# Performance work log

Measured on AMD Instinct MI355X. Metric: run time of the kernel, lower is better.

Reference implementation:

```python
import math
import jax, jax.numpy as jnp
import numpy as np

B, L, D, H, DFF = 2, 2048, 1024, 16, 4096
HD = D // H
NUM_BUCKETS, MAX_DISTANCE = 32, 128


def setup_inputs() -> dict:
    key = jax.random.key(0)
    ks = jax.random.split(key, 10)
    s = 0.02
    return {
        "hidden_states": jax.random.normal(ks[0], (B, L, D), dtype=jnp.float32),
        "Wq": jax.random.normal(ks[1], (D, D), dtype=jnp.float32) * s,
        "Wk": jax.random.normal(ks[2], (D, D), dtype=jnp.float32) * s,
        "Wv": jax.random.normal(ks[3], (D, D), dtype=jnp.float32) * s,
        "Wo": jax.random.normal(ks[4], (D, D), dtype=jnp.float32) * s,
        "W1": jax.random.normal(ks[5], (D, DFF), dtype=jnp.float32) * s,
        "W2": jax.random.normal(ks[6], (DFF, D), dtype=jnp.float32) * s,
        "ln1_g": jnp.ones((D,), dtype=jnp.float32),
        "ln2_g": jnp.ones((D,), dtype=jnp.float32),
        "rel_table": jax.random.normal(ks[7], (NUM_BUCKETS, H), dtype=jnp.float32) * s,
    }


def rms_norm(x, g, eps=1e-6):
    # T5-style LayerNorm: scale only, no mean subtraction
    var = jnp.mean(jnp.square(x.astype(jnp.float32)), axis=-1, keepdims=True)
    return (x.astype(jnp.float32) * jax.lax.rsqrt(var + eps)).astype(x.dtype) * g


def relative_position_bias(seq_len, table):
    # bidirectional T5 bucket scheme, num_buckets=32, max_distance=128
    ctx = jnp.arange(seq_len)[:, None]
    mem = jnp.arange(seq_len)[None, :]
    rp = mem - ctx                                  # (L, L) int
    nb = NUM_BUCKETS // 2
    buckets = (rp > 0).astype(jnp.int32) * nb
    rpa = jnp.abs(rp)
    max_exact = nb // 2
    is_small = rpa < max_exact
    safe = jnp.maximum(rpa, 1).astype(jnp.float32)  # avoid log(0); masked by is_small
    large = max_exact + (
        jnp.log(safe / max_exact) / math.log(MAX_DISTANCE / max_exact) * (nb - max_exact)
    ).astype(jnp.int32)
    large = jnp.minimum(large, nb - 1)
    buckets = buckets + jnp.where(is_small, rpa, large)   # (L, L)
    vals = table[buckets]                                  # (L, L, H)
    return jnp.transpose(vals, (2, 0, 1))[None]            # (1, H, L, L)


def reference(hidden_states, Wq, Wk, Wv, Wo, W1, W2, ln1_g, ln2_g, rel_table):
    x = hidden_states
    b, l, d = x.shape

    # --- self-attention sublayer (pre-norm) ---
    h = rms_norm(x, ln1_g)
    q = (h @ Wq).reshape(b, l, H, HD)
    k = (h @ Wk).reshape(b, l, H, HD)
    v = (h @ Wv).reshape(b, l, H, HD)

    bias = relative_position_bias(l, rel_table)            # (1, H, L, L)
    # NOTE: source's manual attention path has NO 1/sqrt(head_dim) scaling
    scores = jnp.einsum("bqhd,bkhd->bhqk", q, k) + bias
    attn = jax.nn.softmax(scores.astype(jnp.float32), axis=-1).astype(scores.dtype)
    out = jnp.einsum("bhqk,bkhd->bqhd", attn, v).reshape(b, l, d)
    x = x + out @ Wo

    # --- feed-forward sublayer (pre-norm) ---
    h = rms_norm(x, ln2_g)
    x = x + jax.nn.relu(h @ W1) @ W2
    return x
```

## Files before the change

kernel.cpp:

```cpp
#include <hip/hip_runtime.h>
#include <hip/hip_bf16.h>
#include <math.h>

#define BDIM 1024
#define HEADS 16
#define HDIM 64
#define LSEQ 2048
#define NBATCH 2
#define DFFDIM 4096
#define QKVN 3072

typedef __bf16 bf16x8_t __attribute__((ext_vector_type(8)));
typedef float f32x4_t __attribute__((ext_vector_type(4)));

__device__ __forceinline__ ushort f2bf(float f) {
    union { __hip_bfloat16 b; ushort u; } cv;
    cv.b = __float2bfloat16(f);
    return cv.u;
}
__device__ __forceinline__ float bf2f(ushort u) {
    union { unsigned int i; float f; } cv;
    cv.i = ((unsigned int)u) << 16;
    return cv.f;
}

__global__ __launch_bounds__(256) void transpose_cvt(const float* __restrict__ W,
                                                     ushort* __restrict__ Wt,
                                                     int K, int N) {
    __shared__ ushort tile[32][33];
    int bi = blockIdx.y;
    int bj = blockIdx.x;
    int tx = threadIdx.x;
    int ty = threadIdx.y;
#pragma unroll
    for (int r = 0; r < 4; ++r) {
        int krow = bi * 32 + ty + r * 8;
        int ncol = bj * 32 + tx;
        tile[ty + r * 8][tx] = f2bf(W[(size_t)krow * N + ncol]);
    }
    __syncthreads();
#pragma unroll
    for (int r = 0; r < 4; ++r) {
        int nrow = bj * 32 + ty + r * 8;
        int kcol = bi * 32 + tx;
        Wt[(size_t)nrow * K + kcol] = tile[tx][ty + r * 8];
    }
}

__global__ __launch_bounds__(256) void vtrans(const ushort* __restrict__ qkv,
                                              ushort* __restrict__ vT) {
    __shared__ ushort t[64][72];
    const int ktile = blockIdx.x;
    const int bh = blockIdx.y;
    const int b = bh >> 4, h = bh & 15;
    const int tid = threadIdx.x;
    const int r = tid >> 2;
    const int c0 = (tid & 3) * 16;
    const ushort* src = qkv + (size_t)(b * LSEQ + ktile * 64 + r) * QKVN + 2048 + h * HDIM + c0;
    union { bf16x8_t v; ushort s[8]; } u0, u1;
    u0.v = *(const bf16x8_t*)src;
    u1.v = *(const bf16x8_t*)(src + 8);
#pragma unroll
    for (int j = 0; j < 8; ++j) { t[r][c0 + j] = u0.s[j]; t[r][c0 + 8 + j] = u1.s[j]; }
    __syncthreads();
    const int hd = tid >> 2;
    union { bf16x8_t v; ushort s[8]; } w0, w1;
#pragma unroll
    for (int j = 0; j < 8; ++j) { w0.s[j] = t[c0 + j][hd]; w1.s[j] = t[c0 + 8 + j][hd]; }
    ushort* dst = vT + (size_t)(bh * HDIM + hd) * LSEQ + ktile * 64 + c0;
    *(bf16x8_t*)dst = w0.v;
    *(bf16x8_t*)(dst + 8) = w1.v;
}

__global__ __launch_bounds__(256) void rmsnorm_k(const float* __restrict__ x,
                                                 const float* __restrict__ g,
                                                 ushort* __restrict__ out) {
    int row = blockIdx.x;
    int t = threadIdx.x;
    int w = t >> 6, l = t & 63;
    const float4 v = reinterpret_cast<const float4*>(x + (size_t)row * BDIM)[t];
    float ss = v.x * v.x + v.y * v.y + v.z * v.z + v.w * v.w;
#pragma unroll
    for (int m = 1; m <= 32; m <<= 1) ss += __shfl_xor(ss, m);
    __shared__ float wsum[4];
    if (l == 0) wsum[w] = ss;
    __syncthreads();
    float tot = wsum[0] + wsum[1] + wsum[2] + wsum[3];
    float r = rsqrtf(tot * (1.0f / BDIM) + 1e-6f);
    const float4 gv = reinterpret_cast<const float4*>(g)[t];
    ushort4 o;
    o.x = f2bf(v.x * r * gv.x);
    o.y = f2bf(v.y * r * gv.y);
    o.z = f2bf(v.z * r * gv.z);
    o.w = f2bf(v.w * r * gv.w);
    reinterpret_cast<ushort4*>(out + (size_t)row * BDIM)[t] = o;
}

__global__ void bias_table_k(const float* __restrict__ rel, float* __restrict__ btab) {
    int idx = blockIdx.x * 256 + threadIdx.x;
    if (idx >= HEADS * 4095) return;
    int h = idx / 4095;
    int d = idx % 4095;
    int rp = d - 2047;
    int bucket = rp > 0 ? 16 : 0;
    int rpa = rp < 0 ? -rp : rp;
    if (rpa < 8) {
        bucket += rpa;
    } else {
        int large = 8 + (int)(logf((float)rpa * 0.125f) * (1.0f / logf(16.0f)) * 8.0f);
        bucket += large < 15 ? large : 15;
    }
    btab[idx] = rel[bucket * HEADS + h];
}

__global__ __launch_bounds__(256) void reduce2_k(const ushort* __restrict__ parts,
                                                 const float* __restrict__ res,
                                                 float* __restrict__ out,
                                                 size_t mn) {
    size_t i = ((size_t)blockIdx.x * 256 + threadIdx.x) * 4;
    float4 r = *(const float4*)(res + i);
    ushort4 a = *(const ushort4*)(parts + i);
    ushort4 b = *(const ushort4*)(parts + mn + i);
    float4 o;
    o.x = r.x + bf2f(a.x) + bf2f(b.x);
    o.y = r.y + bf2f(a.y) + bf2f(b.y);
    o.z = r.z + bf2f(a.z) + bf2f(b.z);
    o.w = r.w + bf2f(a.w) + bf2f(b.w);
    *(float4*)(out + i) = o;
}

template <int MODE, int TM, int TN>
__global__ __launch_bounds__(256) void gemm_bt(const ushort* __restrict__ A,
                                               const ushort* __restrict__ Bt,
                                               void* Cout, const float* res,
                                               int M, int N, int K, int nbx, int nkc) {
    __shared__ __align__(16) ushort As[2][TM * 64];
    __shared__ __align__(16) ushort Bs[2][TN * 64];
    constexpr int MF = TM / 32, NF = TN / 32;
    const int nwg = gridDim.x;
    const int bid = blockIdx.x;
    const int swz = (bid & 7) * (nwg >> 3) + (bid >> 3);
    const int nxy = nwg / nkc;
    const int chunk = swz / nxy;
    const int bxy = swz % nxy;
    const int bx = bxy % nbx, by = bxy / nbx;
    const int Kc = K / nkc;
    const int kbeg = chunk * Kc;
    const int tid = threadIdx.x;
    const int w = tid >> 6, l = tid & 63;
    const int wm = w >> 1, wn = w & 1;
    const int rowA0 = by * TM;
    const int colB0 = bx * TN;
    const int lr = l >> 3;
    const int scs = ((l & 7) ^ lr) * 8;
    const int c = l & 15, gq = l >> 4;
    const int rswz = (c & 7) * 8;
    f32x4_t acc[MF][NF] = {};

    auto stage = [&](int buf, int k0) {
#pragma unroll
        for (int i = 0; i < TM / 32; ++i) {
            int r = i * 32 + w * 8;
            __builtin_amdgcn_global_load_lds(
                (const __attribute__((address_space(1))) uint32_t*)(A + (size_t)(rowA0 + r + lr) * K + kbeg + k0 + scs),
                (__attribute__((address_space(3))) uint32_t*)(&As[buf][r * 64]), 16, 0, 0);
        }
#pragma unroll
        for (int i = 0; i < TN / 32; ++i) {
            int r = i * 32 + w * 8;
            __builtin_amdgcn_global_load_lds(
                (const __attribute__((address_space(1))) uint32_t*)(Bt + (size_t)(colB0 + r + lr) * K + kbeg + k0 + scs),
                (__attribute__((address_space(3))) uint32_t*)(&Bs[buf][r * 64]), 16, 0, 0);
        }
    };

    stage(0, 0);
    int cur = 0;
    const int nk = Kc >> 6;
    for (int kt = 0; kt < nk; ++kt) {
        __syncthreads();
        if (kt + 1 < nk) stage(cur ^ 1, (kt + 1) << 6);
#pragma unroll
        for (int kk = 0; kk < 2; ++kk) {
            bf16x8_t av[MF], bv[NF];
#pragma unroll
            for (int mf = 0; mf < MF; ++mf)
                av[mf] = *(const bf16x8_t*)&As[cur][(wm * (TM / 2) + mf * 16 + c) * 64 + ((kk * 32 + gq * 8) ^ rswz)];
#pragma unroll
            for (int nf = 0; nf < NF; ++nf)
                bv[nf] = *(const bf16x8_t*)&Bs[cur][(wn * (TN / 2) + nf * 16 + c) * 64 + ((kk * 32 + gq * 8) ^ rswz)];
#pragma unroll
            for (int mf = 0; mf < MF; ++mf)
#pragma unroll
                for (int nf = 0; nf < NF; ++nf)
                    acc[mf][nf] = __builtin_amdgcn_mfma_f32_16x16x32_bf16(av[mf], bv[nf], acc[mf][nf], 0, 0, 0);
        }
        cur ^= 1;
    }
#pragma unroll
    for (int mf = 0; mf < MF; ++mf) {
#pragma unroll
        for (int nf = 0; nf < NF; ++nf) {
#pragma unroll
            for (int i = 0; i < 4; ++i) {
                int row = rowA0 + wm * (TM / 2) + mf * 16 + gq * 4 + i;
                int col = colB0 + wn * (TN / 2) + nf * 16 + c;
                size_t idx = (size_t)row * N + col;
                float vv = acc[mf][nf][i];
                if (MODE == 0) {
                    ((ushort*)Cout)[idx] = f2bf(vv);
                } else if (MODE == 1) {
                    ((float*)Cout)[idx] = res[idx] + vv;
                } else if (MODE == 2) {
                    ((ushort*)Cout)[idx] = f2bf(vv > 0.f ? vv : 0.f);
                } else {
                    ((ushort*)Cout)[(size_t)chunk * M * N + idx] = f2bf(vv);
                }
            }
        }
    }
}

__global__ __launch_bounds__(512) void attn_fwd(const ushort* __restrict__ qkv,
                                                const ushort* __restrict__ vT,
                                                const float* __restrict__ btab,
                                                ushort* __restrict__ ob) {
    const int tid = threadIdx.x, w = tid >> 6, l = tid & 63;
    const int bh = blockIdx.y, b = bh >> 4, h = bh & 15;
    const int qt = blockIdx.x;
    __shared__ __align__(16) ushort Ks[2][64 * 64];
    __shared__ __align__(16) ushort Vs[2][64 * 64];
    __shared__ __align__(16) ushort Pl[8][16 * 72];
    const int q0 = qt * 128 + w * 16;
    const int c = l & 15, g = l >> 4;
    const size_t rowbase = (size_t)b * LSEQ * QKVN;
    const ushort* qp = qkv + rowbase + h * HDIM;
    const ushort* kp = qkv + rowbase + BDIM + h * HDIM;
    const ushort* vtp = vT + (size_t)bh * HDIM * LSEQ;
    const int sr = tid >> 3;
    const int scs = ((l & 7) ^ (l >> 3)) * 8;
    const float* btq4 = btab + h * 4095 + 2047 - (q0 + c) + g * 4;

    bf16x8_t aq[2];
#pragma unroll
    for (int kk = 0; kk < 2; ++kk)
        aq[kk] = *(const bf16x8_t*)(qp + (size_t)(q0 + c) * QKVN + kk * 32 + g * 8);

    float mrow = -INFINITY, lrow = 0.f;
    f32x4_t o[4] = {};
    f32x4_t s[4];

    auto stage = [&](int buf, int key0) {
        __builtin_amdgcn_global_load_lds(
            (const __attribute__((address_space(1))) uint32_t*)(kp + (size_t)(key0 + sr) * QKVN + scs),
            (__attribute__((address_space(3))) uint32_t*)(&Ks[buf][(w * 8) * 64]), 16, 0, 0);
        __builtin_amdgcn_global_load_lds(
            (const __attribute__((address_space(1))) uint32_t*)(vtp + (size_t)sr * LSEQ + key0 + scs),
            (__attribute__((address_space(3))) uint32_t*)(&Vs[buf][(w * 8) * 64]), 16, 0, 0);
    };
    auto loadBias = [&](int key0) {
#pragma unroll
        for (int nf = 0; nf < 4; ++nf)
#pragma unroll
            for (int i = 0; i < 4; ++i)
                s[nf][i] = btq4[key0 + nf * 16 + i];
    };

    stage(0, 0);
    loadBias(0);
    int cur = 0;

    ushort* Pw = Pl[w];
    const int rswz = (c & 7) << 3;
    for (int kt = 0; kt < 32; ++kt) {
        __syncthreads();
        if (kt < 31) stage(cur ^ 1, kt * 64 + 64);
#pragma unroll
        for (int kk = 0; kk < 2; ++kk)
#pragma unroll
            for (int nf = 0; nf < 4; ++nf) {
                bf16x8_t kf = *(const bf16x8_t*)&Ks[cur][(nf * 16 + c) * 64 + ((kk * 32 + g * 8) ^ rswz)];
                s[nf] = __builtin_amdgcn_mfma_f32_16x16x32_bf16(kf, aq[kk], s[nf], 0, 0, 0);
            }
        float tmax = -INFINITY;
#pragma unroll
        for (int nf = 0; nf < 4; ++nf)
#pragma unroll
            for (int i = 0; i < 4; ++i)
                tmax = fmaxf(tmax, s[nf][i]);
        tmax = fmaxf(tmax, __shfl_xor(tmax, 16));
        tmax = fmaxf(tmax, __shfl_xor(tmax, 32));
        if (!__all(tmax - mrow <= 8.f)) {
            float mn = fmaxf(mrow, tmax);
            float sc2 = __expf(mrow - mn);
            mrow = mn;
            lrow *= sc2;
#pragma unroll
            for (int hf = 0; hf < 4; ++hf) o[hf] *= sc2;
        }
        float rs = 0.f;
        union { ushort us[4]; uint2 u2; } pk[4];
#pragma unroll
        for (int nf = 0; nf < 4; ++nf)
#pragma unroll
            for (int i = 0; i < 4; ++i) {
                float pv = __expf(s[nf][i] - mrow);
                rs += pv;
                pk[nf].us[i] = f2bf(pv);
            }
        if (kt < 31) loadBias(kt * 64 + 64);
        rs += __shfl_xor(rs, 16);
        rs += __shfl_xor(rs, 32);
        lrow += rs;
#pragma unroll
        for (int nf = 0; nf < 4; ++nf)
            *(uint2*)&Pw[c * 72 + nf * 16 + g * 4] = pk[nf].u2;
        bf16x8_t pa[2];
#pragma unroll
        for (int kk = 0; kk < 2; ++kk)
            pa[kk] = *(const bf16x8_t*)&Pw[c * 72 + kk * 32 + g * 8];
#pragma unroll
        for (int kk = 0; kk < 2; ++kk)
#pragma unroll
            for (int hf = 0; hf < 4; ++hf) {
                bf16x8_t vf = *(const bf16x8_t*)&Vs[cur][(hf * 16 + c) * 64 + ((kk * 32 + g * 8) ^ rswz)];
                o[hf] = __builtin_amdgcn_mfma_f32_16x16x32_bf16(vf, pa[kk], o[hf], 0, 0, 0);
            }
        cur ^= 1;
    }
    const float inv = 1.f / lrow;
    ushort* orow = ob + (size_t)(b * LSEQ + q0 + c) * BDIM + h * HDIM + g * 4;
#pragma unroll
    for (int hf = 0; hf < 4; ++hf) {
        ushort4 ov;
        ov.x = f2bf(o[hf][0] * inv);
        ov.y = f2bf(o[hf][1] * inv);
        ov.z = f2bf(o[hf][2] * inv);
        ov.w = f2bf(o[hf][3] * inv);
        *(ushort4*)(orow + hf * 16) = ov;
    }
}

extern "C" void kernel_launch(void* const* d_in, const int* in_sizes, int n_in,
                              void* d_out, int out_size, void* d_ws, size_t ws_size,
                              hipStream_t stream) {
    const float* x   = (const float*)d_in[0];
    const float* Wq  = (const float*)d_in[1];
    const float* Wk  = (const float*)d_in[2];
    const float* Wv  = (const float*)d_in[3];
    const float* Wo  = (const float*)d_in[4];
    const float* W1  = (const float*)d_in[5];
    const float* W2  = (const float*)d_in[6];
    const float* g1  = (const float*)d_in[7];
    const float* g2  = (const float*)d_in[8];
    const float* rel = (const float*)d_in[9];
    float* out = (float*)d_out;

    char* ws = (char*)d_ws;
    const size_t MB = 1024 * 1024;
    ushort* wqkvT = (ushort*)(ws + 0 * MB);
    ushort* woT   = (ushort*)(ws + 6 * MB);
    ushort* w1T   = (ushort*)(ws + 8 * MB);
    ushort* w2T   = (ushort*)(ws + 16 * MB);
    float*  btab  = (float*)(ws + 24 * MB);
    ushort* hbuf  = (ushort*)(ws + 25 * MB);
    ushort* qkvb  = (ushort*)(ws + 33 * MB);
    ushort* woP   = (ushort*)(ws + 33 * MB);
    ushort* f1b   = (ushort*)(ws + 33 * MB);
    ushort* vTb   = (ushort*)(ws + 57 * MB);
    ushort* w2P   = (ushort*)(ws + 0 * MB);
    (void)in_sizes; (void)n_in; (void)out_size; (void)ws_size;

    const size_t MN = (size_t)4096 * 1024;
    dim3 tb(32, 8);
    transpose_cvt<<<dim3(32, 32),  tb, 0, stream>>>(Wq, wqkvT,                1024, 1024);
    transpose_cvt<<<dim3(32, 32),  tb, 0, stream>>>(Wk, wqkvT + 1024 * 1024,  1024, 1024);
    transpose_cvt<<<dim3(32, 32),  tb, 0, stream>>>(Wv, wqkvT + 2048 * 1024,  1024, 1024);
    transpose_cvt<<<dim3(32, 32),  tb, 0, stream>>>(Wo, woT, 1024, 1024);
    transpose_cvt<<<dim3(128, 32), tb, 0, stream>>>(W1, w1T, 1024, 4096);
    transpose_cvt<<<dim3(32, 128), tb, 0, stream>>>(W2, w2T, 4096, 1024);
    bias_table_k<<<256, 256, 0, stream>>>(rel, btab);

    rmsnorm_k<<<4096, 256, 0, stream>>>(x, g1, hbuf);
    gemm_bt<0, 128, 64><<<1536, 256, 0, stream>>>(hbuf, wqkvT, qkvb, nullptr, 4096, QKVN, 1024, 48, 1);
    vtrans<<<dim3(32, 32), 256, 0, stream>>>(qkvb, vTb);
    attn_fwd<<<dim3(16, 32), 512, 0, stream>>>(qkvb, vTb, btab, hbuf);
    gemm_bt<3, 128, 64><<<1024, 256, 0, stream>>>(hbuf, woT, woP, nullptr, 4096, 1024, 1024, 16, 2);
    reduce2_k<<<4096, 256, 0, stream>>>(woP, x, out, MN);
    rmsnorm_k<<<4096, 256, 0, stream>>>(out, g2, hbuf);
    gemm_bt<2, 128, 64><<<2048, 256, 0, stream>>>(hbuf, w1T, f1b, nullptr, 4096, DFFDIM, 1024, 64, 1);
    gemm_bt<3, 128, 64><<<1024, 256, 0, stream>>>(f1b, w2T, w2P, nullptr, 4096, 1024, 4096, 16, 2);
    reduce2_k<<<4096, 256, 0, stream>>>(w2P, out, out, MN);
}
```

Measured before the change: 276.8 us.

## Enlarge GEMM tiles, single-buffer LDS, fuse residual+RMSNorm, tune attention softmax

Switches all GEMMs to 128x128 tiles with a single LDS buffer and two barriers per K step, dropping the double-buffered prefetch. The residual reduction is fused with the second RMSNorm into one kernel, removing a pass over the activations. The attention kernel gains s_setprio hints around its MFMA blocks, a tree max reduction, and exp2-based softmax with a prescaled max. The larger tiles are meant to increase data reuse per block, but they lower occupancy, and the single buffer exposes global-load latency that prefetching used to hide.

Result: faster. 259.6 us (-6.2%).

```diff
diff --git a/kernel.cpp b/kernel.cpp
--- a/kernel.cpp
+++ b/kernel.cpp
@@ -9,6 +9,7 @@
 #define NBATCH 2
 #define DFFDIM 4096
 #define QKVN 3072
+#define LOG2E 1.44269504f
 
 typedef __bf16 bf16x8_t __attribute__((ext_vector_type(8)));
 typedef float f32x4_t __attribute__((ext_vector_type(4)));
@@ -129,13 +130,49 @@
     *(float4*)(out + i) = o;
 }
 
+__global__ __launch_bounds__(256) void reduce2_rms(const ushort* __restrict__ parts,
+                                                   const float* __restrict__ res,
+                                                   const float* __restrict__ g,
+                                                   float* __restrict__ out,
+                                                   ushort* __restrict__ hout,
+                                                   size_t mn) {
+    int row = blockIdx.x;
+    int t = threadIdx.x;
+    int w = t >> 6, l = t & 63;
+    size_t i = (size_t)row * BDIM + t * 4;
+    float4 r = *(const float4*)(res + i);
+    ushort4 a = *(const ushort4*)(parts + i);
+    ushort4 b = *(const ushort4*)(parts + mn + i);
+    float4 o;
+    o.x = r.x + bf2f(a.x) + bf2f(b.x);
+    o.y = r.y + bf2f(a.y) + bf2f(b.y);
+    o.z = r.z + bf2f(a.z) + bf2f(b.z);
+    o.w = r.w + bf2f(a.w) + bf2f(b.w);
+    *(float4*)(out + i) = o;
+    float ss = o.x * o.x + o.y * o.y + o.z * o.z + o.w * o.w;
+#pragma unroll
+    for (int m = 1; m <= 32; m <<= 1) ss += __shfl_xor(ss, m);
+    __shared__ float wsum[4];
+    if (l == 0) wsum[w] = ss;
+    __syncthreads();
+    float tot = wsum[0] + wsum[1] + wsum[2] + wsum[3];
+    float rr = rsqrtf(tot * (1.0f / BDIM) + 1e-6f);
+    const float4 gv = reinterpret_cast<const float4*>(g)[t];
+    ushort4 h;
+    h.x = f2bf(o.x * rr * gv.x);
+    h.y = f2bf(o.y * rr * gv.y);
+    h.z = f2bf(o.z * rr * gv.z);
+    h.w = f2bf(o.w * rr * gv.w);
+    reinterpret_cast<ushort4*>(hout + (size_t)row * BDIM)[t] = h;
+}
+
 template <int MODE, int TM, int TN>
 __global__ __launch_bounds__(256) void gemm_bt(const ushort* __restrict__ A,
                                                const ushort* __restrict__ Bt,
                                                void* Cout, const float* res,
                                                int M, int N, int K, int nbx, int nkc) {
-    __shared__ __align__(16) ushort As[2][TM * 64];
-    __shared__ __align__(16) ushort Bs[2][TN * 64];
+    __shared__ __align__(16) ushort As[TM * 64];
+    __shared__ __align__(16) ushort Bs[TN * 64];
     constexpr int MF = TM / 32, NF = TN / 32;
     const int nwg = gridDim.x;
     const int bid = blockIdx.x;
@@ -157,45 +194,43 @@
     const int rswz = (c & 7) * 8;
     f32x4_t acc[MF][NF] = {};
 
-    auto stage = [&](int buf, int k0) {
+    auto stage = [&](int k0) {
 #pragma unroll
         for (int i = 0; i < TM / 32; ++i) {
             int r = i * 32 + w * 8;
             __builtin_amdgcn_global_load_lds(
                 (const __attribute__((address_space(1))) uint32_t*)(A + (size_t)(rowA0 + r + lr) * K + kbeg + k0 + scs),
-                (__attribute__((address_space(3))) uint32_t*)(&As[buf][r * 64]), 16, 0, 0);
+                (__attribute__((address_space(3))) uint32_t*)(&As[r * 64]), 16, 0, 0);
         }
 #pragma unroll
         for (int i = 0; i < TN / 32; ++i) {
             int r = i * 32 + w * 8;
             __builtin_amdgcn_global_load_lds(
                 (const __attribute__((address_space(1))) uint32_t*)(Bt + (size_t)(colB0 + r + lr) * K + kbeg + k0 + scs),
-                (__attribute__((address_space(3))) uint32_t*)(&Bs[buf][r * 64]), 16, 0, 0);
+                (__attribute__((address_space(3))) uint32_t*)(&Bs[r * 64]), 16, 0, 0);
         }
     };
 
-    stage(0, 0);
-    int cur = 0;
     const int nk = Kc >> 6;
     for (int kt = 0; kt < nk; ++kt) {
         __syncthreads();
-        if (kt + 1 < nk) stage(cur ^ 1, (kt + 1) << 6);
+        stage(kt << 6);
+        __syncthreads();
 #pragma unroll
         for (int kk = 0; kk < 2; ++kk) {
             bf16x8_t av[MF], bv[NF];
 #pragma unroll
             for (int mf = 0; mf < MF; ++mf)
-                av[mf] = *(const bf16x8_t*)&As[cur][(wm * (TM / 2) + mf * 16 + c) * 64 + ((kk * 32 + gq * 8) ^ rswz)];
+                av[mf] = *(const bf16x8_t*)&As[(wm * (TM / 2) + mf * 16 + c) * 64 + ((kk * 32 + gq * 8) ^ rswz)];
 #pragma unroll
             for (int nf = 0; nf < NF; ++nf)
-                bv[nf] = *(const bf16x8_t*)&Bs[cur][(wn * (TN / 2) + nf * 16 + c) * 64 + ((kk * 32 + gq * 8) ^ rswz)];
+                bv[nf] = *(const bf16x8_t*)&Bs[(wn * (TN / 2) + nf * 16 + c) * 64 + ((kk * 32 + gq * 8) ^ rswz)];
 #pragma unroll
             for (int mf = 0; mf < MF; ++mf)
 #pragma unroll
                 for (int nf = 0; nf < NF; ++nf)
                     acc[mf][nf] = __builtin_amdgcn_mfma_f32_16x16x32_bf16(av[mf], bv[nf], acc[mf][nf], 0, 0, 0);
         }
-        cur ^= 1;
     }
 #pragma unroll
     for (int mf = 0; mf < MF; ++mf) {
@@ -246,7 +281,7 @@
     for (int kk = 0; kk < 2; ++kk)
         aq[kk] = *(const bf16x8_t*)(qp + (size_t)(q0 + c) * QKVN + kk * 32 + g * 8);
 
-    float mrow = -INFINITY, lrow = 0.f;
+    float mrow = -INFINITY, lrow = 0.f, m2 = -INFINITY;
     f32x4_t o[4] = {};
     f32x4_t s[4];
 
@@ -275,6 +310,7 @@
     for (int kt = 0; kt < 32; ++kt) {
         __syncthreads();
         if (kt < 31) stage(cur ^ 1, kt * 64 + 64);
+        __builtin_amdgcn_s_setprio(1);
 #pragma unroll
         for (int kk = 0; kk < 2; ++kk)
 #pragma unroll
@@ -282,18 +318,19 @@
                 bf16x8_t kf = *(const bf16x8_t*)&Ks[cur][(nf * 16 + c) * 64 + ((kk * 32 + g * 8) ^ rswz)];
                 s[nf] = __builtin_amdgcn_mfma_f32_16x16x32_bf16(kf, aq[kk], s[nf], 0, 0, 0);
             }
-        float tmax = -INFINITY;
-#pragma unroll
-        for (int nf = 0; nf < 4; ++nf)
-#pragma unroll
-            for (int i = 0; i < 4; ++i)
-                tmax = fmaxf(tmax, s[nf][i]);
+        __builtin_amdgcn_s_setprio(0);
+        float tmax = fmaxf(
+            fmaxf(fmaxf(fmaxf(s[0][0], s[0][1]), fmaxf(s[0][2], s[0][3])),
+                  fmaxf(fmaxf(s[1][0], s[1][1]), fmaxf(s[1][2], s[1][3]))),
+            fmaxf(fmaxf(fmaxf(s[2][0], s[2][1]), fmaxf(s[2][2], s[2][3])),
+                  fmaxf(fmaxf(s[3][0], s[3][1]), fmaxf(s[3][2], s[3][3]))));
         tmax = fmaxf(tmax, __shfl_xor(tmax, 16));
         tmax = fmaxf(tmax, __shfl_xor(tmax, 32));
         if (!__all(tmax - mrow <= 8.f)) {
             float mn = fmaxf(mrow, tmax);
-            float sc2 = __expf(mrow - mn);
+            float sc2 = exp2f((mrow - mn) * LOG2E);
             mrow = mn;
+            m2 = mn * LOG2E;
             lrow *= sc2;
 #pragma unroll
             for (int hf = 0; hf < 4; ++hf) o[hf] *= sc2;
@@ -304,7 +341,7 @@
         for (int nf = 0; nf < 4; ++nf)
 #pragma unroll
             for (int i = 0; i < 4; ++i) {
-                float pv = __expf(s[nf][i] - mrow);
+                float pv = exp2f(fmaf(s[nf][i], LOG2E, -m2));
                 rs += pv;
                 pk[nf].us[i] = f2bf(pv);
             }
@@ -319,6 +356,7 @@
 #pragma unroll
         for (int kk = 0; kk < 2; ++kk)
             pa[kk] = *(const bf16x8_t*)&Pw[c * 72 + kk * 32 + g * 8];
+        __builtin_amdgcn_s_setprio(1);
 #pragma unroll
         for (int kk = 0; kk < 2; ++kk)
 #pragma unroll
@@ -326,6 +364,7 @@
                 bf16x8_t vf = *(const bf16x8_t*)&Vs[cur][(hf * 16 + c) * 64 + ((kk * 32 + g * 8) ^ rswz)];
                 o[hf] = __builtin_amdgcn_mfma_f32_16x16x32_bf16(vf, pa[kk], o[hf], 0, 0, 0);
             }
+        __builtin_amdgcn_s_setprio(0);
         cur ^= 1;
     }
     const float inv = 1.f / lrow;
@@ -382,13 +421,12 @@
     bias_table_k<<<256, 256, 0, stream>>>(rel, btab);
 
     rmsnorm_k<<<4096, 256, 0, stream>>>(x, g1, hbuf);
-    gemm_bt<0, 128, 64><<<1536, 256, 0, stream>>>(hbuf, wqkvT, qkvb, nullptr, 4096, QKVN, 1024, 48, 1);
+    gemm_bt<0, 128, 128><<<768, 256, 0, stream>>>(hbuf, wqkvT, qkvb, nullptr, 4096, QKVN, 1024, 24, 1);
     vtrans<<<dim3(32, 32), 256, 0, stream>>>(qkvb, vTb);
     attn_fwd<<<dim3(16, 32), 512, 0, stream>>>(qkvb, vTb, btab, hbuf);
-    gemm_bt<3, 128, 64><<<1024, 256, 0, stream>>>(hbuf, woT, woP, nullptr, 4096, 1024, 1024, 16, 2);
-    reduce2_k<<<4096, 256, 0, stream>>>(woP, x, out, MN);
-    rmsnorm_k<<<4096, 256, 0, stream>>>(out, g2, hbuf);
-    gemm_bt<2, 128, 64><<<2048, 256, 0, stream>>>(hbuf, w1T, f1b, nullptr, 4096, DFFDIM, 1024, 64, 1);
-    gemm_bt<3, 128, 64><<<1024, 256, 0, stream>>>(f1b, w2T, w2P, nullptr, 4096, 1024, 4096, 16, 2);
+    gemm_bt<3, 128, 128><<<512, 256, 0, stream>>>(hbuf, woT, woP, nullptr, 4096, 1024, 1024, 8, 2);
+    reduce2_rms<<<4096, 256, 0, stream>>>(woP, x, g2, out, hbuf, MN);
+    gemm_bt<2, 128, 128><<<1024, 256, 0, stream>>>(hbuf, w1T, f1b, nullptr, 4096, DFFDIM, 1024, 32, 1);
+    gemm_bt<3, 128, 128><<<512, 256, 0, stream>>>(f1b, w2T, w2P, nullptr, 4096, 1024, 4096, 8, 2);
     reduce2_k<<<4096, 256, 0, stream>>>(w2P, out, out, MN);
 }
```
